# Kernel optimization log

Hardware: AMD Instinct MI355X
Metric: run time of the kernel (lower is better)

The kernel has to match this reference:

```python
import jax, jax.numpy as jnp
import numpy as np

B, N, D, E, H = 8, 256, 128, 32, 4
HD = D // H
EPS = 1e-5


def setup_inputs() -> dict:
    key = jax.random.key(0)
    ks = jax.random.split(key, 20)
    idx = jnp.arange(N)

    h = jax.random.normal(ks[0], (B, N, D), dtype=jnp.float32)
    adj = (jax.random.uniform(ks[1], (B, N, N)) < 0.5).astype(jnp.float32)
    adj = adj.at[:, idx, idx].set(1.0)
    edge_features = jax.random.normal(ks[2], (B, N, N, E), dtype=jnp.float32)
    src_mask = (jax.random.uniform(ks[3], (B, N, N)) < 0.7).astype(jnp.float32)
    src_mask = src_mask.at[:, idx, idx].set(1.0)

    s = 1.0 / np.sqrt(D)
    se = 1.0 / np.sqrt(E)
    p = {
        "gcn_w": jax.random.normal(ks[4], (D, D)) * s,
        "gcn_b": jnp.zeros((D,)),
        "edge_w": jax.random.normal(ks[5], (D, E)) * se,
        "edge_b": jnp.zeros((D,)),
        "wq": jax.random.normal(ks[6], (D, D)) * s,
        "wk": jax.random.normal(ks[7], (D, D)) * s,
        "wv": jax.random.normal(ks[8], (D, D)) * s,
        "bq": jnp.zeros((D,)),
        "bk": jnp.zeros((D,)),
        "bv": jnp.zeros((D,)),
        "out_w": jax.random.normal(ks[9], (D, D)) * s,
        "out_b": jnp.zeros((D,)),
        "ln_g": jnp.ones((D,)),
        "ln_b": jnp.zeros((D,)),
    }
    return {"h": h, "adj": adj, "edge_features": edge_features, "src_mask": src_mask, **p}


def reference(h, adj, edge_features, src_mask,
              gcn_w, gcn_b, edge_w, edge_b,
              wq, wk, wv, bq, bk, bv, out_w, out_b, ln_g, ln_b):
    b, n, d = h.shape

    # --- GCN branch: degree-normalized aggregation with self-loops ---
    adj_sl = adj + jnp.eye(n, dtype=h.dtype)[None]          # (B,N,N)
    deg = adj_sl.sum(-1, keepdims=True)                      # (B,N,1)
    h_agg = jnp.einsum('bnm,bmd->bnd', adj_sl, h) / deg
    h_gcn = h_agg @ gcn_w.T + gcn_b                          # (B,N,D)

    # --- edge-conditioned key/value: h_ij = h_j + edge_emb ---
    edge_emb = jnp.einsum('bnme,de->bnmd', edge_features, edge_w) + edge_b
    h_ij = h[:, None, :, :] + edge_emb                       # (B,N,N,D)

    # key padding mask: True where edge absent (masked)
    masked = (adj * src_mask) == 0                           # (B,N,N)

    # --- multi-head attention, one query per node ---
    q = (h @ wq.T + bq).reshape(b, n, H, HD)                 # (B,N,H,HD)
    k = (jnp.einsum('bnmd,ed->bnme', h_ij, wk) + bk).reshape(b, n, n, H, HD)
    v = (jnp.einsum('bnmd,ed->bnme', h_ij, wv) + bv).reshape(b, n, n, H, HD)

    scores = jnp.einsum('bnhd,bnmhd->bnhm', q, k) / np.sqrt(HD)  # (B,N,H,N)
    scores = jnp.where(masked[:, :, None, :], -jnp.inf, scores)
    attn = jax.nn.softmax(scores, axis=-1)
    o = jnp.einsum('bnhm,bnmhd->bnhd', attn, v).reshape(b, n, d)
    o = o @ out_w.T + out_b                                  # (B,N,D)

    # residual + layernorm (dropout is identity in eval)
    x = h + o
    mu = x.mean(-1, keepdims=True)
    var = ((x - mu) ** 2).mean(-1, keepdims=True)
    h_attn = ln_g * (x - mu) / jnp.sqrt(var + EPS) + ln_b

    return h_gcn + h_attn
```

## Files before the change

### kernel.cpp

```cpp
#include <hip/hip_runtime.h>
#include <hip/hip_bf16.h>

#define OFF_WQT 0
#define OFF_WKT 16384
#define OFF_WVT 32768
#define OFF_OWT 49152
#define OFF_GWT 65536
#define OFF_WKE 81920
#define OFF_WVE 86016
#define OFF_KB  90112
#define OFF_VB  90240
#define OFF_SC  90368
#define OFF_QS  98560
#define OFF_QE  360704
#define OFF_O   884992
#define OFF_K0  1147136
#define OFF_V0  1278208

static __device__ __forceinline__ float bflo(unsigned int w){
  union { unsigned int u; float f; } x; x.u = w << 16; return x.f;
}
static __device__ __forceinline__ float bfhi(unsigned int w){
  union { unsigned int u; float f; } x; x.u = w & 0xffff0000u; return x.f;
}
static __device__ __forceinline__ unsigned short f2bf(float f){
  union { float f; unsigned int u; } x; x.f = f;
  unsigned int r = (x.u + 0x7fffu + ((x.u >> 16) & 1u)) >> 16;
  return (unsigned short)r;
}

__global__ __launch_bounds__(256) void prep_kernel(
    const float* __restrict__ wq, const float* __restrict__ wk,
    const float* __restrict__ wv, const float* __restrict__ out_w,
    const float* __restrict__ gcn_w, const float* __restrict__ edge_w,
    const float* __restrict__ edge_b, const float* __restrict__ bk,
    const float* __restrict__ bv, float* __restrict__ ws)
{
  int blk = blockIdx.x, t = threadIdx.x;
  if (blk < 320) {
    int w = blk >> 6;
    int e0 = (blk & 63) * 256 + t;
    const float* src = (w==0) ? wq : (w==1) ? wk : (w==2) ? wv : (w==3) ? out_w : gcn_w;
    float* dst = ws + ((w==0) ? OFF_WQT : (w==1) ? OFF_WKT : (w==2) ? OFF_WVT
                      : (w==3) ? OFF_OWT : OFF_GWT);
    int k = e0 >> 7, d = e0 & 127;
    dst[e0] = src[d*128 + k];
  } else if (blk < 352) {
    int idx = blk - 320;
    int which = idx >> 4;
    int e0 = (idx & 15) * 256 + t;
    int d = e0 >> 5, e = e0 & 31;
    const float* W = which ? wv : wk;
    float acc = 0.f;
    #pragma unroll 4
    for (int k2 = 0; k2 < 128; ++k2) acc += W[d*128+k2] * edge_w[k2*32+e];
    ws[(which ? OFF_WVE : OFF_WKE) + e0] = acc;
  } else {
    int d = t & 127;
    const float* W  = (t < 128) ? wk : wv;
    const float* bb = (t < 128) ? bk : bv;
    float acc = bb[d];
    #pragma unroll 4
    for (int k2 = 0; k2 < 128; ++k2) acc += W[d*128+k2] * edge_b[k2];
    ws[((t < 128) ? OFF_KB : OFF_VB) + d] = acc;
  }
}

__global__ __launch_bounds__(256) void proj_kernel(
    const float* __restrict__ h, const float* __restrict__ bq,
    float* __restrict__ ws)
{
  __shared__ float h_lds[512];
  __shared__ float p1[2][4][128];
  __shared__ float p2[2][4][128];
  __shared__ float p3[2][4][128];
  __shared__ float qrow[4*132];

  int t = threadIdx.x;
  int d = t & 127;
  int kh = t >> 7;
  int r0 = blockIdx.x * 4;

  if (t < 128) ((float4*)h_lds)[t] = ((const float4*)(h + (size_t)r0*128))[t];
  __syncthreads();

  const float* wqT = ws + OFF_WQT;
  const float* wkT = ws + OFF_WKT;
  const float* wvT = ws + OFF_WVT;

  float aq[4] = {0,0,0,0};
  float ak[4] = {0,0,0,0};
  float av[4] = {0,0,0,0};

  for (int kk = 0; kk < 64; ++kk) {
    int k = kh*64 + kk;
    float qw = wqT[k*128 + d];
    float kw = wkT[k*128 + d];
    float vw = wvT[k*128 + d];
    #pragma unroll
    for (int i = 0; i < 4; ++i) {
      float hv = h_lds[i*128 + k];
      aq[i] += qw * hv;
      ak[i] += kw * hv;
      av[i] += vw * hv;
    }
  }
  #pragma unroll
  for (int i = 0; i < 4; ++i) {
    p1[kh][i][d] = aq[i];
    p2[kh][i][d] = ak[i];
    p3[kh][i][d] = av[i];
  }
  __syncthreads();

  unsigned short* K0 = (unsigned short*)(ws + OFF_K0);
  unsigned short* V0 = (unsigned short*)(ws + OFF_V0);
  if (t < 128) {
    const float inv = 0.17677669529663687f;
    #pragma unroll
    for (int i = 0; i < 4; ++i) {
      float q  = (p1[0][i][d] + p1[1][i][d] + bq[d]) * inv;
      float k0 = p2[0][i][d] + p2[1][i][d];
      float v0 = p3[0][i][d] + p3[1][i][d];
      ws[OFF_QS + (size_t)(r0+i)*128 + d] = q;
      qrow[i*132 + d] = q;
      K0[(size_t)(r0+i)*128 + d] = f2bf(k0);
      V0[(size_t)(r0+i)*128 + d] = f2bf(v0);
    }
  }
  __syncthreads();

  const float* Wke = ws + OFF_WKE;
  #pragma unroll
  for (int rep = 0; rep < 2; ++rep) {
    int flat = rep*256 + t;
    int i = flat >> 7, he = flat & 127;
    int hh = he >> 5, e = he & 31;
    float acc = 0.f;
    #pragma unroll
    for (int j = 0; j < 32; ++j)
      acc += Wke[(hh*32+j)*32 + e] * qrow[i*132 + hh*32 + j];
    ws[OFF_QE + (size_t)(r0+i)*128 + he] = acc;
  }
  if (t < 16) {
    int i = t >> 2, hh = t & 3;
    float acc = 0.f;
    #pragma unroll
    for (int j = 0; j < 32; ++j)
      acc += qrow[i*132 + hh*32 + j] * ws[OFF_KB + hh*32 + j];
    ws[OFF_SC + (size_t)(r0+i)*4 + hh] = acc;
  }
}

__global__ __launch_bounds__(256, 4) void attn_kernel(
    const float* __restrict__ edge, const float* __restrict__ adj,
    const float* __restrict__ srcm, const float* __restrict__ ws,
    float* __restrict__ obuf)
{
  __shared__ unsigned int e_bf[256*18];
  __shared__ float s_lds[1028];
  __shared__ float part4[8*132];
  __shared__ float part5[8*132];
  __shared__ float ebar[128];
  __shared__ float red[8];

  int t  = threadIdx.x;
  int bn = blockIdx.x;
  int b  = bn >> 8;

  const float* qs = ws + OFF_QS + (size_t)bn*128;
  const float* qe = ws + OFF_QE + (size_t)bn*128;
  const float* sc = ws + OFF_SC + (size_t)bn*4;
  const unsigned short* K0 = (const unsigned short*)(ws + OFF_K0);
  const unsigned int*  V0u = (const unsigned int*)(ws + OFF_V0);

  int m = t;
  float ma = adj[(size_t)bn*256 + m];
  float msk = srcm[(size_t)bn*256 + m];
  float4 ev[8];
  {
    const float4* ep = (const float4*)(edge + ((size_t)bn*256 + (size_t)m)*32);
    #pragma unroll
    for (int j = 0; j < 8; ++j) ev[j] = ep[j];
    unsigned int* erow = e_bf + m*18;
    #pragma unroll
    for (int j = 0; j < 8; ++j) {
      uint2 pk;
      pk.x = (unsigned int)f2bf(ev[j].x) | ((unsigned int)f2bf(ev[j].y) << 16);
      pk.y = (unsigned int)f2bf(ev[j].z) | ((unsigned int)f2bf(ev[j].w) << 16);
      *(uint2*)(erow + j*2) = pk;
    }
  }

  float s4[4];
  {
    const uint4* kv = (const uint4*)(K0 + (size_t)(b*256 + m)*128);
    #pragma unroll
    for (int hh = 0; hh < 4; ++hh) {
      float acc = sc[hh];
      #pragma unroll
      for (int q4 = 0; q4 < 4; ++q4) {
        uint4 kw = kv[hh*4 + q4];
        const float* qp = qs + hh*32 + q4*8;
        acc += qp[0]*bflo(kw.x) + qp[1]*bfhi(kw.x)
             + qp[2]*bflo(kw.y) + qp[3]*bfhi(kw.y)
             + qp[4]*bflo(kw.z) + qp[5]*bfhi(kw.z)
             + qp[6]*bflo(kw.w) + qp[7]*bfhi(kw.w);
      }
      const float* qep = qe + hh*32;
      #pragma unroll
      for (int j = 0; j < 8; ++j) {
        acc += qep[4*j+0]*ev[j].x + qep[4*j+1]*ev[j].y
             + qep[4*j+2]*ev[j].z + qep[4*j+3]*ev[j].w;
      }
      s4[hh] = acc;
    }
    if (ma * msk == 0.0f) { s4[0] = s4[1] = s4[2] = s4[3] = -1e30f; }
    #pragma unroll
    for (int hh = 0; hh < 4; ++hh) s_lds[hh*257 + m] = s4[hh];
  }
  __syncthreads();

  {
    int wvh = t >> 6, ln = t & 63;
    float v0 = s_lds[wvh*257 + ln];
    float v1 = s_lds[wvh*257 + ln + 64];
    float v2 = s_lds[wvh*257 + ln + 128];
    float v3 = s_lds[wvh*257 + ln + 192];
    float mx = fmaxf(fmaxf(v0, v1), fmaxf(v2, v3));
    #pragma unroll
    for (int off = 32; off > 0; off >>= 1) mx = fmaxf(mx, __shfl_down(mx, off));
    mx = __shfl(mx, 0);
    float sm = __expf(v0-mx) + __expf(v1-mx) + __expf(v2-mx) + __expf(v3-mx);
    #pragma unroll
    for (int off = 32; off > 0; off >>= 1) sm += __shfl_down(sm, off);
    if (ln == 0) { red[wvh] = mx; red[4+wvh] = 1.0f / sm; }
  }
  __syncthreads();

  #pragma unroll
  for (int hh = 0; hh < 4; ++hh)
    s_lds[hh*257 + m] = __expf(s4[hh] - red[hh]) * red[4+hh];
  __syncthreads();

  {
    int ms  = t >> 5;
    int hh4 = (t >> 3) & 3, e4 = t & 7;
    int c   = t & 31,  hh5 = c >> 3;
    float p4x=0,p4y=0,p4z=0,p4w=0;
    float p5x=0,p5y=0,p5z=0,p5w=0;
    const unsigned int* vrow = V0u + (size_t)b*256*64;
    for (int jm = 0; jm < 32; ++jm) {
      int mm = ms*32 + jm;
      float a4 = s_lds[hh4*257 + mm];
      uint2 w = *(const uint2*)(e_bf + mm*18 + e4*2);
      p4x += a4*bflo(w.x); p4y += a4*bfhi(w.x);
      p4z += a4*bflo(w.y); p4w += a4*bfhi(w.y);
      float a5 = s_lds[hh5*257 + mm];
      uint2 vv = *(const uint2*)(vrow + (size_t)mm*64 + c*2);
      p5x += a5*bflo(vv.x); p5y += a5*bfhi(vv.x);
      p5z += a5*bflo(vv.y); p5w += a5*bfhi(vv.y);
    }
    float4 f4; f4.x=p4x; f4.y=p4y; f4.z=p4z; f4.w=p4w;
    *(float4*)(part4 + ms*132 + hh4*32 + e4*4) = f4;
    float4 f5; f5.x=p5x; f5.y=p5y; f5.z=p5z; f5.w=p5w;
    *(float4*)(part5 + ms*132 + c*4) = f5;
  }
  __syncthreads();

  float s2 = 0.f;
  if (t < 128) {
    float se = 0.f;
    #pragma unroll
    for (int g = 0; g < 8; ++g) { se += part4[g*132 + t]; s2 += part5[g*132 + t]; }
    ebar[t] = se;
  }
  __syncthreads();

  if (t < 128) {
    int hh = t >> 5;
    float acc = s2 + ws[OFF_VB + t];
    const float* wve = ws + OFF_WVE + t*32;
    #pragma unroll
    for (int e = 0; e < 32; ++e) acc += wve[e] * ebar[hh*32 + e];
    obuf[(size_t)bn*128 + t] = acc;
  }
}

__global__ __launch_bounds__(256) void final_kernel(
    const float* __restrict__ h, const float* __restrict__ adj,
    const float* __restrict__ ws, const float* __restrict__ out_b,
    const float* __restrict__ ln_g, const float* __restrict__ ln_b,
    const float* __restrict__ gcn_b, float* __restrict__ out)
{
  __shared__ float adj_lds[1024];
  __shared__ float o_lds[512];
  __shared__ float ha_lds[4*132];
  __shared__ float pa[2][4][128];
  __shared__ float pb[2][4][128];
  __shared__ float dpart[2][4];
  __shared__ float xl[4*132];
  __shared__ float stat[8];

  int t = threadIdx.x;
  int d = t & 127;
  int kh = t >> 7;
  int b  = blockIdx.x >> 6;
  int n0 = (blockIdx.x & 63) * 4;
  int r0 = b*256 + n0;

  ((float4*)adj_lds)[t] = ((const float4*)(adj + (size_t)r0*256))[t];
  if (t < 128) ((float4*)o_lds)[t] = ((const float4*)(ws + OFF_O + (size_t)r0*128))[t];
  __syncthreads();

  {
    float ag[4] = {0,0,0,0};
    float dg[4] = {0,0,0,0};
    for (int mm = 0; mm < 128; ++mm) {
      int mloc = kh*128 + mm;
      float hv = h[((size_t)b*256 + mloc)*128 + d];
      #pragma unroll
      for (int i = 0; i < 4; ++i) {
        float a = adj_lds[i*256 + mloc] + ((mloc == n0 + i) ? 1.0f : 0.0f);
        ag[i] += a * hv;
        dg[i] += a;
      }
    }
    #pragma unroll
    for (int i = 0; i < 4; ++i) pa[kh][i][d] = ag[i];
    if (d == 0) {
      #pragma unroll
      for (int i = 0; i < 4; ++i) dpart[kh][i] = dg[i];
    }
  }
  __syncthreads();
  if (t < 128) {
    #pragma unroll
    for (int i = 0; i < 4; ++i)
      ha_lds[i*132 + d] = (pa[0][i][d] + pa[1][i][d]) / (dpart[0][i] + dpart[1][i]);
  }
  __syncthreads();

  {
    const float* owT = ws + OFF_OWT;
    const float* gwT = ws + OFF_GWT;
    float xa[4] = {0,0,0,0};
    float ga[4] = {0,0,0,0};
    for (int kk = 0; kk < 64; ++kk) {
      int k = kh*64 + kk;
      float ow = owT[k*128 + d];
      float gw = gwT[k*128 + d];
      #pragma unroll
      for (int i = 0; i < 4; ++i) {
        xa[i] += ow * o_lds[i*128 + k];
        ga[i] += gw * ha_lds[i*132 + k];
      }
    }
    #pragma unroll
    for (int i = 0; i < 4; ++i) { pa[kh][i][d] = xa[i]; pb[kh][i][d] = ga[i]; }
  }
  __syncthreads();

  float gtot[4];
  if (t < 128) {
    #pragma unroll
    for (int i = 0; i < 4; ++i) {
      float x = pa[0][i][d] + pa[1][i][d] + out_b[d] + h[(size_t)(r0+i)*128 + d];
      xl[i*132 + d] = x;
      gtot[i] = pb[0][i][d] + pb[1][i][d];
    }
  }
  __syncthreads();

  {
    int i = t >> 6, l = t & 63;
    float x0 = xl[i*132 + l];
    float x1 = xl[i*132 + l + 64];
    float s = x0 + x1, ss = x0*x0 + x1*x1;
    #pragma unroll
    for (int off = 32; off > 0; off >>= 1) {
      s  += __shfl_down(s,  off);
      ss += __shfl_down(ss, off);
    }
    if (l == 0) {
      float mu  = s * (1.0f/128.0f);
      float var = ss * (1.0f/128.0f) - mu*mu;
      stat[i]   = mu;
      stat[4+i] = rsqrtf(var + 1e-5f);
    }
  }
  __syncthreads();

  if (t < 128) {
    #pragma unroll
    for (int i = 0; i < 4; ++i) {
      float x = xl[i*132 + d];
      out[(size_t)(r0+i)*128 + d] =
          ln_g[d]*(x - stat[i])*stat[4+i] + ln_b[d] + gtot[i] + gcn_b[d];
    }
  }
}

extern "C" void kernel_launch(void* const* d_in, const int* in_sizes, int n_in,
                              void* d_out, int out_size, void* d_ws, size_t ws_size,
                              hipStream_t stream) {
  (void)in_sizes; (void)n_in; (void)out_size; (void)ws_size;
  const float* h     = (const float*)d_in[0];
  const float* adj   = (const float*)d_in[1];
  const float* edge  = (const float*)d_in[2];
  const float* srcm  = (const float*)d_in[3];
  const float* gcn_w = (const float*)d_in[4];
  const float* gcn_b = (const float*)d_in[5];
  const float* edge_w= (const float*)d_in[6];
  const float* edge_b= (const float*)d_in[7];
  const float* wq    = (const float*)d_in[8];
  const float* wk    = (const float*)d_in[9];
  const float* wv    = (const float*)d_in[10];
  const float* bq    = (const float*)d_in[11];
  const float* bk    = (const float*)d_in[12];
  const float* bv    = (const float*)d_in[13];
  const float* out_w = (const float*)d_in[14];
  const float* out_b = (const float*)d_in[15];
  const float* ln_g  = (const float*)d_in[16];
  const float* ln_b  = (const float*)d_in[17];

  float* ws  = (float*)d_ws;
  float* out = (float*)d_out;

  prep_kernel<<<353, 256, 0, stream>>>(wq, wk, wv, out_w, gcn_w, edge_w, edge_b, bk, bv, ws);
  proj_kernel<<<512, 256, 0, stream>>>(h, bq, ws);
  attn_kernel<<<2048, 256, 0, stream>>>(edge, adj, srcm, ws, ws + OFF_O);
  final_kernel<<<512, 256, 0, stream>>>(h, adj, ws, out_b, ln_g, ln_b, gcn_b, out);
}
```

Baseline: 197.5 us.

## Fuse four kernels into two: merge prep/GCN into proj, epilogue into attention

Reduces the pipeline from four launches to two. Weight transposes are dropped in favour of row-major float4 weight reads. The Wke/bias prep work moves into the first blocks of the projection kernel, and the GCN aggregation and projection move there too. The q·Wke/score-bias computation, output projection, residual and layernorm move into the attention kernel. Edge tiles are now loaded coalesced into LDS, and the occupancy hint is raised to 5. This cuts launch overhead and intermediate round-trips, at the cost of recomputing the out_w matvec per row without reuse across rows. There is also an apparent race: the proj blocks write Wke/KB while other proj blocks in the same launch may not need them, and attn reads them only after the launch, so ordering is fine.

```diff
diff --git a/kernel.cpp b/kernel.cpp
--- a/kernel.cpp
+++ b/kernel.cpp
@@ -1,21 +1,14 @@
 #include <hip/hip_runtime.h>
 #include <hip/hip_bf16.h>
 
-#define OFF_WQT 0
-#define OFF_WKT 16384
-#define OFF_WVT 32768
-#define OFF_OWT 49152
-#define OFF_GWT 65536
-#define OFF_WKE 81920
-#define OFF_WVE 86016
-#define OFF_KB  90112
-#define OFF_VB  90240
-#define OFF_SC  90368
-#define OFF_QS  98560
-#define OFF_QE  360704
-#define OFF_O   884992
-#define OFF_K0  1147136
-#define OFF_V0  1278208
+#define OFF_WKE 0
+#define OFF_WVE 4096
+#define OFF_KB  8192
+#define OFF_VB  8320
+#define OFF_QS  8448
+#define OFF_HG  270592
+#define OFF_K0  532736
+#define OFF_V0  663808
 
 static __device__ __forceinline__ float bflo(unsigned int w){
   union { unsigned int u; float f; } x; x.u = w << 16; return x.f;
@@ -23,196 +16,227 @@
 static __device__ __forceinline__ float bfhi(unsigned int w){
   union { unsigned int u; float f; } x; x.u = w & 0xffff0000u; return x.f;
 }
-static __device__ __forceinline__ unsigned short f2bf(float f){
+static __device__ __forceinline__ unsigned int f2bf(float f){
   union { float f; unsigned int u; } x; x.f = f;
-  unsigned int r = (x.u + 0x7fffu + ((x.u >> 16) & 1u)) >> 16;
-  return (unsigned short)r;
-}
-
-__global__ __launch_bounds__(256) void prep_kernel(
+  return (x.u + 0x7fffu + ((x.u >> 16) & 1u)) >> 16;
+}
+
+__global__ __launch_bounds__(256) void proj_kernel(
+    const float* __restrict__ h, const float* __restrict__ adj,
+    const float* __restrict__ gcn_w, const float* __restrict__ gcn_b,
+    const float* __restrict__ edge_w, const float* __restrict__ edge_b,
     const float* __restrict__ wq, const float* __restrict__ wk,
-    const float* __restrict__ wv, const float* __restrict__ out_w,
-    const float* __restrict__ gcn_w, const float* __restrict__ edge_w,
-    const float* __restrict__ edge_b, const float* __restrict__ bk,
-    const float* __restrict__ bv, float* __restrict__ ws)
+    const float* __restrict__ wv, const float* __restrict__ bq,
+    const float* __restrict__ bk, const float* __restrict__ bv,
+    float* __restrict__ ws)
 {
-  int blk = blockIdx.x, t = threadIdx.x;
-  if (blk < 320) {
-    int w = blk >> 6;
-    int e0 = (blk & 63) * 256 + t;
-    const float* src = (w==0) ? wq : (w==1) ? wk : (w==2) ? wv : (w==3) ? out_w : gcn_w;
-    float* dst = ws + ((w==0) ? OFF_WQT : (w==1) ? OFF_WKT : (w==2) ? OFF_WVT
-                      : (w==3) ? OFF_OWT : OFF_GWT);
-    int k = e0 >> 7, d = e0 & 127;
-    dst[e0] = src[d*128 + k];
-  } else if (blk < 352) {
-    int idx = blk - 320;
-    int which = idx >> 4;
-    int e0 = (idx & 15) * 256 + t;
-    int d = e0 >> 5, e = e0 & 31;
+  __shared__ float h_lds[4*128];
+  __shared__ float adj_lds[4*256];
+  __shared__ float p1[2][4][128];
+  __shared__ float p2[2][4][128];
+  __shared__ float p3[2][4][128];
+  __shared__ float ha_lds[4*132];
+  __shared__ float dpart[2][4];
+
+  int t = threadIdx.x;
+  int d = t & 127, kh = t >> 7;
+  int b = blockIdx.x >> 6;
+  int n0 = (blockIdx.x & 63) * 4;
+  int r0 = b*256 + n0;
+
+  if (t < 128) ((float4*)h_lds)[t] = ((const float4*)(h + (size_t)r0*128))[t];
+  ((float4*)adj_lds)[t] = ((const float4*)(adj + (size_t)r0*256))[t];
+  __syncthreads();
+
+  {
+    const float4* wq4 = (const float4*)(wq + (size_t)d*128 + kh*64);
+    const float4* wk4 = (const float4*)(wk + (size_t)d*128 + kh*64);
+    const float4* wv4 = (const float4*)(wv + (size_t)d*128 + kh*64);
+    float aq[4]={0,0,0,0}, ak[4]={0,0,0,0}, av[4]={0,0,0,0};
+    #pragma unroll
+    for (int kk = 0; kk < 16; ++kk) {
+      float4 qw = wq4[kk], kw = wk4[kk], vw = wv4[kk];
+      int k0 = kh*64 + kk*4;
+      #pragma unroll
+      for (int i = 0; i < 4; ++i) {
+        const float* hr = h_lds + i*128 + k0;
+        aq[i] += qw.x*hr[0] + qw.y*hr[1] + qw.z*hr[2] + qw.w*hr[3];
+        ak[i] += kw.x*hr[0] + kw.y*hr[1] + kw.z*hr[2] + kw.w*hr[3];
+        av[i] += vw.x*hr[0] + vw.y*hr[1] + vw.z*hr[2] + vw.w*hr[3];
+      }
+    }
+    #pragma unroll
+    for (int i = 0; i < 4; ++i) { p1[kh][i][d]=aq[i]; p2[kh][i][d]=ak[i]; p3[kh][i][d]=av[i]; }
+  }
+  __syncthreads();
+
+  unsigned short* K0 = (unsigned short*)(ws + OFF_K0);
+  unsigned short* V0 = (unsigned short*)(ws + OFF_V0);
+  if (t < 128) {
+    const float inv = 0.17677669529663687f;
+    #pragma unroll
+    for (int i = 0; i < 4; ++i) {
+      ws[OFF_QS + (size_t)(r0+i)*128 + d] = (p1[0][i][d] + p1[1][i][d] + bq[d]) * inv;
+      K0[(size_t)(r0+i)*128 + d] = (unsigned short)f2bf(p2[0][i][d] + p2[1][i][d]);
+      V0[(size_t)(r0+i)*128 + d] = (unsigned short)f2bf(p3[0][i][d] + p3[1][i][d]);
+    }
+  }
+  __syncthreads();
+
+  {
+    float ag[4]={0,0,0,0}, dg[4]={0,0,0,0};
+    for (int mm = 0; mm < 128; ++mm) {
+      int ml = kh*128 + mm;
+      float hv = h[((size_t)b*256 + ml)*128 + d];
+      #pragma unroll
+      for (int i = 0; i < 4; ++i) {
+        float a = adj_lds[i*256 + ml] + ((ml == n0 + i) ? 1.0f : 0.0f);
+        ag[i] += a * hv;
+        dg[i] += a;
+      }
+    }
+    #pragma unroll
+    for (int i = 0; i < 4; ++i) p1[kh][i][d] = ag[i];
+    if (d == 0) {
+      #pragma unroll
+      for (int i = 0; i < 4; ++i) dpart[kh][i] = dg[i];
+    }
+  }
+  __syncthreads();
+  if (t < 128) {
+    #pragma unroll
+    for (int i = 0; i < 4; ++i)
+      ha_lds[i*132 + d] = (p1[0][i][d] + p1[1][i][d]) / (dpart[0][i] + dpart[1][i]);
+  }
+  __syncthreads();
+
+  {
+    const float4* gw4 = (const float4*)(gcn_w + (size_t)d*128 + kh*64);
+    float ga[4]={0,0,0,0};
+    #pragma unroll
+    for (int kk = 0; kk < 16; ++kk) {
+      float4 g4 = gw4[kk];
+      int k0 = kh*64 + kk*4;
+      #pragma unroll
+      for (int i = 0; i < 4; ++i) {
+        const float* hr = ha_lds + i*132 + k0;
+        ga[i] += g4.x*hr[0] + g4.y*hr[1] + g4.z*hr[2] + g4.w*hr[3];
+      }
+    }
+    #pragma unroll
+    for (int i = 0; i < 4; ++i) p2[kh][i][d] = ga[i];
+  }
+  __syncthreads();
+  if (t < 128) {
+    #pragma unroll
+    for (int i = 0; i < 4; ++i)
+      ws[OFF_HG + (size_t)(r0+i)*128 + d] = p2[0][i][d] + p2[1][i][d] + gcn_b[d];
+  }
+
+  if (blockIdx.x < 32) {
+    int which = blockIdx.x >> 4;
+    int e0 = (blockIdx.x & 15) * 256 + t;
+    int dd = e0 >> 5, e = e0 & 31;
     const float* W = which ? wv : wk;
     float acc = 0.f;
     #pragma unroll 4
-    for (int k2 = 0; k2 < 128; ++k2) acc += W[d*128+k2] * edge_w[k2*32+e];
+    for (int k2 = 0; k2 < 128; ++k2) acc += W[dd*128+k2] * edge_w[k2*32+e];
     ws[(which ? OFF_WVE : OFF_WKE) + e0] = acc;
-  } else {
-    int d = t & 127;
+  } else if (blockIdx.x == 32) {
+    int dd = t & 127;
     const float* W  = (t < 128) ? wk : wv;
     const float* bb = (t < 128) ? bk : bv;
-    float acc = bb[d];
+    float acc = bb[dd];
     #pragma unroll 4
-    for (int k2 = 0; k2 < 128; ++k2) acc += W[d*128+k2] * edge_b[k2];
-    ws[((t < 128) ? OFF_KB : OFF_VB) + d] = acc;
-  }
-}
-
-__global__ __launch_bounds__(256) void proj_kernel(
-    const float* __restrict__ h, const float* __restrict__ bq,
-    float* __restrict__ ws)
-{
-  __shared__ float h_lds[512];
-  __shared__ float p1[2][4][128];
-  __shared__ float p2[2][4][128];
-  __shared__ float p3[2][4][128];
-  __shared__ float qrow[4*132];
-
-  int t = threadIdx.x;
-  int d = t & 127;
-  int kh = t >> 7;
-  int r0 = blockIdx.x * 4;
-
-  if (t < 128) ((float4*)h_lds)[t] = ((const float4*)(h + (size_t)r0*128))[t];
-  __syncthreads();
-
-  const float* wqT = ws + OFF_WQT;
-  const float* wkT = ws + OFF_WKT;
-  const float* wvT = ws + OFF_WVT;
-
-  float aq[4] = {0,0,0,0};
-  float ak[4] = {0,0,0,0};
-  float av[4] = {0,0,0,0};
-
-  for (int kk = 0; kk < 64; ++kk) {
-    int k = kh*64 + kk;
-    float qw = wqT[k*128 + d];
-    float kw = wkT[k*128 + d];
-    float vw = wvT[k*128 + d];
-    #pragma unroll
-    for (int i = 0; i < 4; ++i) {
-      float hv = h_lds[i*128 + k];
-      aq[i] += qw * hv;
-      ak[i] += kw * hv;
-      av[i] += vw * hv;
-    }
-  }
-  #pragma unroll
-  for (int i = 0; i < 4; ++i) {
-    p1[kh][i][d] = aq[i];
-    p2[kh][i][d] = ak[i];
-    p3[kh][i][d] = av[i];
-  }
-  __syncthreads();
-
-  unsigned short* K0 = (unsigned short*)(ws + OFF_K0);
-  unsigned short* V0 = (unsigned short*)(ws + OFF_V0);
-  if (t < 128) {
-    const float inv = 0.17677669529663687f;
-    #pragma unroll
-    for (int i = 0; i < 4; ++i) {
-      float q  = (p1[0][i][d] + p1[1][i][d] + bq[d]) * inv;
-      float k0 = p2[0][i][d] + p2[1][i][d];
-      float v0 = p3[0][i][d] + p3[1][i][d];
-      ws[OFF_QS + (size_t)(r0+i)*128 + d] = q;
-      qrow[i*132 + d] = q;
-      K0[(size_t)(r0+i)*128 + d] = f2bf(k0);
-      V0[(size_t)(r0+i)*128 + d] = f2bf(v0);
-    }
-  }
-  __syncthreads();
-
-  const float* Wke = ws + OFF_WKE;
-  #pragma unroll
-  for (int rep = 0; rep < 2; ++rep) {
-    int flat = rep*256 + t;
-    int i = flat >> 7, he = flat & 127;
-    int hh = he >> 5, e = he & 31;
-    float acc = 0.f;
-    #pragma unroll
-    for (int j = 0; j < 32; ++j)
-      acc += Wke[(hh*32+j)*32 + e] * qrow[i*132 + hh*32 + j];
-    ws[OFF_QE + (size_t)(r0+i)*128 + he] = acc;
-  }
-  if (t < 16) {
-    int i = t >> 2, hh = t & 3;
-    float acc = 0.f;
-    #pragma unroll
-    for (int j = 0; j < 32; ++j)
-      acc += qrow[i*132 + hh*32 + j] * ws[OFF_KB + hh*32 + j];
-    ws[OFF_SC + (size_t)(r0+i)*4 + hh] = acc;
-  }
-}
-
-__global__ __launch_bounds__(256, 4) void attn_kernel(
+    for (int k2 = 0; k2 < 128; ++k2) acc += W[dd*128+k2] * edge_b[k2];
+    ws[((t < 128) ? OFF_KB : OFF_VB) + dd] = acc;
+  }
+}
+
+__global__ __launch_bounds__(256, 5) void attn_kernel(
     const float* __restrict__ edge, const float* __restrict__ adj,
-    const float* __restrict__ srcm, const float* __restrict__ ws,
-    float* __restrict__ obuf)
+    const float* __restrict__ srcm, const float* __restrict__ h,
+    const float* __restrict__ out_w, const float* __restrict__ out_b,
+    const float* __restrict__ ln_g, const float* __restrict__ ln_b,
+    const float* __restrict__ ws, float* __restrict__ out)
 {
   __shared__ unsigned int e_bf[256*18];
   __shared__ float s_lds[1028];
   __shared__ float part4[8*132];
   __shared__ float part5[8*132];
   __shared__ float ebar[128];
+  __shared__ float qs_l[128];
+  __shared__ float qe_l[128];
+  __shared__ float sc_l[4];
   __shared__ float red[8];
 
   int t  = threadIdx.x;
   int bn = blockIdx.x;
   int b  = bn >> 8;
 
-  const float* qs = ws + OFF_QS + (size_t)bn*128;
-  const float* qe = ws + OFF_QE + (size_t)bn*128;
-  const float* sc = ws + OFF_SC + (size_t)bn*4;
-  const unsigned short* K0 = (const unsigned short*)(ws + OFF_K0);
-  const unsigned int*  V0u = (const unsigned int*)(ws + OFF_V0);
+  {
+    const float4* et = (const float4*)(edge + (size_t)bn*8192);
+    #pragma unroll
+    for (int it = 0; it < 8; ++it) {
+      int fi = it*256 + t;
+      float4 v = et[fi];
+      int row = fi >> 3, c4 = fi & 7;
+      uint2 pk;
+      pk.x = f2bf(v.x) | (f2bf(v.y) << 16);
+      pk.y = f2bf(v.z) | (f2bf(v.w) << 16);
+      *(uint2*)(e_bf + row*18 + c4*2) = pk;
+    }
+  }
+  float ma  = adj[(size_t)bn*256 + t];
+  float msk = srcm[(size_t)bn*256 + t];
+  if (t < 128) qs_l[t] = ws[OFF_QS + (size_t)bn*128 + t];
+  __syncthreads();
+
+  if (t < 128) {
+    int hh = t >> 5, e = t & 31;
+    float acc = 0.f;
+    #pragma unroll
+    for (int j = 0; j < 32; ++j)
+      acc += ws[OFF_WKE + (hh*32 + j)*32 + e] * qs_l[hh*32 + j];
+    qe_l[t] = acc;
+  } else if (t < 132) {
+    int hh = t - 128;
+    float acc = 0.f;
+    #pragma unroll
+    for (int j = 0; j < 32; ++j)
+      acc += qs_l[hh*32 + j] * ws[OFF_KB + hh*32 + j];
+    sc_l[hh] = acc;
+  }
+  __syncthreads();
 
   int m = t;
-  float ma = adj[(size_t)bn*256 + m];
-  float msk = srcm[(size_t)bn*256 + m];
-  float4 ev[8];
-  {
-    const float4* ep = (const float4*)(edge + ((size_t)bn*256 + (size_t)m)*32);
-    #pragma unroll
-    for (int j = 0; j < 8; ++j) ev[j] = ep[j];
-    unsigned int* erow = e_bf + m*18;
+  float s4[4];
+  {
+    float e32[32];
+    const uint2* er = (const uint2*)(e_bf + m*18);
     #pragma unroll
     for (int j = 0; j < 8; ++j) {
-      uint2 pk;
-      pk.x = (unsigned int)f2bf(ev[j].x) | ((unsigned int)f2bf(ev[j].y) << 16);
-      pk.y = (unsigned int)f2bf(ev[j].z) | ((unsigned int)f2bf(ev[j].w) << 16);
-      *(uint2*)(erow + j*2) = pk;
-    }
-  }
-
-  float s4[4];
-  {
-    const uint4* kv = (const uint4*)(K0 + (size_t)(b*256 + m)*128);
+      uint2 w = er[j];
+      e32[4*j+0] = bflo(w.x); e32[4*j+1] = bfhi(w.x);
+      e32[4*j+2] = bflo(w.y); e32[4*j+3] = bfhi(w.y);
+    }
+    const uint4* kv = (const uint4*)((const unsigned short*)(ws + OFF_K0)
+                                     + (size_t)(b*256 + m)*128);
     #pragma unroll
     for (int hh = 0; hh < 4; ++hh) {
-      float acc = sc[hh];
+      float acc = sc_l[hh];
       #pragma unroll
       for (int q4 = 0; q4 < 4; ++q4) {
         uint4 kw = kv[hh*4 + q4];
-        const float* qp = qs + hh*32 + q4*8;
+        const float* qp = qs_l + hh*32 + q4*8;
         acc += qp[0]*bflo(kw.x) + qp[1]*bfhi(kw.x)
              + qp[2]*bflo(kw.y) + qp[3]*bfhi(kw.y)
              + qp[4]*bflo(kw.z) + qp[5]*bfhi(kw.z)
              + qp[6]*bflo(kw.w) + qp[7]*bfhi(kw.w);
       }
-      const float* qep = qe + hh*32;
-      #pragma unroll
-      for (int j = 0; j < 8; ++j) {
-        acc += qep[4*j+0]*ev[j].x + qep[4*j+1]*ev[j].y
-             + qep[4*j+2]*ev[j].z + qep[4*j+3]*ev[j].w;
-      }
+      const float* qep = qe_l + hh*32;
+      #pragma unroll
+      for (int j = 0; j < 32; ++j) acc += qep[j]*e32[j];
       s4[hh] = acc;
     }
     if (ma * msk == 0.0f) { s4[0] = s4[1] = s4[2] = s4[3] = -1e30f; }
@@ -249,7 +273,7 @@
     int c   = t & 31,  hh5 = c >> 3;
     float p4x=0,p4y=0,p4z=0,p4w=0;
     float p5x=0,p5y=0,p5z=0,p5w=0;
-    const unsigned int* vrow = V0u + (size_t)b*256*64;
+    const unsigned int* vrow = (const unsigned int*)(ws + OFF_V0) + (size_t)b*256*64;
     for (int jm = 0; jm < 32; ++jm) {
       int mm = ms*32 + jm;
       float a4 = s_lds[hh4*257 + mm];
@@ -280,124 +304,55 @@
   if (t < 128) {
     int hh = t >> 5;
     float acc = s2 + ws[OFF_VB + t];
-    const float* wve = ws + OFF_WVE + t*32;
+    const float* wve = ws + OFF_WVE + (size_t)t*32;
     #pragma unroll
     for (int e = 0; e < 32; ++e) acc += wve[e] * ebar[hh*32 + e];
-    obuf[(size_t)bn*128 + t] = acc;
-  }
-}
-
-__global__ __launch_bounds__(256) void final_kernel(
-    const float* __restrict__ h, const float* __restrict__ adj,
-    const float* __restrict__ ws, const float* __restrict__ out_b,
-    const float* __restrict__ ln_g, const float* __restrict__ ln_b,
-    const float* __restrict__ gcn_b, float* __restrict__ out)
-{
-  __shared__ float adj_lds[1024];
-  __shared__ float o_lds[512];
-  __shared__ float ha_lds[4*132];
-  __shared__ float pa[2][4][128];
-  __shared__ float pb[2][4][128];
-  __shared__ float dpart[2][4];
-  __shared__ float xl[4*132];
-  __shared__ float stat[8];
-
-  int t = threadIdx.x;
-  int d = t & 127;
-  int kh = t >> 7;
-  int b  = blockIdx.x >> 6;
-  int n0 = (blockIdx.x & 63) * 4;
-  int r0 = b*256 + n0;
-
-  ((float4*)adj_lds)[t] = ((const float4*)(adj + (size_t)r0*256))[t];
-  if (t < 128) ((float4*)o_lds)[t] = ((const float4*)(ws + OFF_O + (size_t)r0*128))[t];
-  __syncthreads();
-
-  {
-    float ag[4] = {0,0,0,0};
-    float dg[4] = {0,0,0,0};
-    for (int mm = 0; mm < 128; ++mm) {
-      int mloc = kh*128 + mm;
-      float hv = h[((size_t)b*256 + mloc)*128 + d];
-      #pragma unroll
-      for (int i = 0; i < 4; ++i) {
-        float a = adj_lds[i*256 + mloc] + ((mloc == n0 + i) ? 1.0f : 0.0f);
-        ag[i] += a * hv;
-        dg[i] += a;
-      }
-    }
-    #pragma unroll
-    for (int i = 0; i < 4; ++i) pa[kh][i][d] = ag[i];
-    if (d == 0) {
-      #pragma unroll
-      for (int i = 0; i < 4; ++i) dpart[kh][i] = dg[i];
-    }
-  }
-  __syncthreads();
-  if (t < 128) {
-    #pragma unroll
-    for (int i = 0; i < 4; ++i)
-      ha_lds[i*132 + d] = (pa[0][i][d] + pa[1][i][d]) / (dpart[0][i] + dpart[1][i]);
-  }
-  __syncthreads();
-
-  {
-    const float* owT = ws + OFF_OWT;
-    const float* gwT = ws + OFF_GWT;
-    float xa[4] = {0,0,0,0};
-    float ga[4] = {0,0,0,0};
-    for (int kk = 0; kk < 64; ++kk) {
-      int k = kh*64 + kk;
-      float ow = owT[k*128 + d];
-      float gw = gwT[k*128 + d];
-      #pragma unroll
-      for (int i = 0; i < 4; ++i) {
-        xa[i] += ow * o_lds[i*128 + k];
-        ga[i] += gw * ha_lds[i*132 + k];
-      }
-    }
-    #pragma unroll
-    for (int i = 0; i < 4; ++i) { pa[kh][i][d] = xa[i]; pb[kh][i][d] = ga[i]; }
-  }
-  __syncthreads();
-
-  float gtot[4];
-  if (t < 128) {
-    #pragma unroll
-    for (int i = 0; i < 4; ++i) {
-      float x = pa[0][i][d] + pa[1][i][d] + out_b[d] + h[(size_t)(r0+i)*128 + d];
-      xl[i*132 + d] = x;
-      gtot[i] = pb[0][i][d] + pb[1][i][d];
-    }
-  }
-  __syncthreads();
-
-  {
-    int i = t >> 6, l = t & 63;
-    float x0 = xl[i*132 + l];
-    float x1 = xl[i*132 + l + 64];
+    part4[t] = acc;
+  }
+  float hv = (t < 128) ? h[(size_t)bn*128 + t] : 0.f;
+  __syncthreads();
+
+  {
+    int d = t & 127, kh = t >> 7;
+    const float4* ow4 = (const float4*)(out_w + (size_t)d*128 + kh*64);
+    float xa = 0.f;
+    #pragma unroll
+    for (int kk = 0; kk < 16; ++kk) {
+      float4 w4 = ow4[kk];
+      const float* op = part4 + kh*64 + kk*4;
+      xa += w4.x*op[0] + w4.y*op[1] + w4.z*op[2] + w4.w*op[3];
+    }
+    part5[kh*128 + d] = xa;
+  }
+  __syncthreads();
+
+  float x = 0.f;
+  if (t < 128) {
+    x = part5[t] + part5[128 + t] + out_b[t] + hv;
+    part4[256 + t] = x;
+  }
+  __syncthreads();
+
+  if (t < 64) {
+    float x0 = part4[256 + t], x1 = part4[256 + t + 64];
     float s = x0 + x1, ss = x0*x0 + x1*x1;
     #pragma unroll
     for (int off = 32; off > 0; off >>= 1) {
       s  += __shfl_down(s,  off);
       ss += __shfl_down(ss, off);
     }
-    if (l == 0) {
-      float mu  = s * (1.0f/128.0f);
-      float var = ss * (1.0f/128.0f) - mu*mu;
-      stat[i]   = mu;
-      stat[4+i] = rsqrtf(var + 1e-5f);
-    }
-  }
-  __syncthreads();
-
-  if (t < 128) {
-    #pragma unroll
-    for (int i = 0; i < 4; ++i) {
-      float x = xl[i*132 + d];
-      out[(size_t)(r0+i)*128 + d] =
-          ln_g[d]*(x - stat[i])*stat[4+i] + ln_b[d] + gtot[i] + gcn_b[d];
-    }
+    if (t == 0) {
+      float mu = s * (1.0f/128.0f);
+      red[0] = mu;
+      red[1] = rsqrtf(ss * (1.0f/128.0f) - mu*mu + 1e-5f);
+    }
+  }
+  __syncthreads();
+
+  if (t < 128) {
+    float mu = red[0], rs = red[1];
+    out[(size_t)bn*128 + t] =
+        ln_g[t]*(x - mu)*rs + ln_b[t] + ws[OFF_HG + (size_t)bn*128 + t];
   }
 }
 
@@ -427,8 +382,8 @@
   float* ws  = (float*)d_ws;
   float* out = (float*)d_out;
 
-  prep_kernel<<<353, 256, 0, stream>>>(wq, wk, wv, out_w, gcn_w, edge_w, edge_b, bk, bv, ws);
-  proj_kernel<<<512, 256, 0, stream>>>(h, bq, ws);
-  attn_kernel<<<2048, 256, 0, stream>>>(edge, adj, srcm, ws, ws + OFF_O);
-  final_kernel<<<512, 256, 0, stream>>>(h, adj, ws, out_b, ln_g, ln_b, gcn_b, out);
-}
+  proj_kernel<<<512, 256, 0, stream>>>(h, adj, gcn_w, gcn_b, edge_w, edge_b,
+                                       wq, wk, wv, bq, bk, bv, ws);
+  attn_kernel<<<2048, 256, 0, stream>>>(edge, adj, srcm, h, out_w, out_b,
+                                        ln_g, ln_b, ws, out);
+}
```

New measurement: 206.3 us. 1.04x slower.
